# Performance work log

Measured on AMD Instinct MI355X. Metric: run time of the kernel, lower is better.

## Reference

```python
import jax, jax.numpy as jnp
import numpy as np

WEIGHTS = (0.5, 1.0, 2.0)   # per-channel weights (init kwarg)
INVERTED = True             # init kwarg


def setup_inputs() -> dict:
    key = jax.random.key(0)
    B, C, H, W = 16, 3, 256, 256
    # binary flood mask: nonzero = foreground (scipy EDT measures distance to nearest zero)
    flood = jax.random.randint(key, (B, C, H, W), 0, 2).astype(jnp.float32)
    return {"flood_batch": flood}


def _edt_squared(mask):
    """Exact squared Euclidean distance transform per [H,W] slice.

    mask: bool [B,C,H,W], True = foreground (nonzero). Returns float32 [B,C,H,W]
    squared distance from each True pixel to the nearest False pixel (0 at False).
    Uses the exact separable decomposition:
      D2[r,w] = min_{r'} ( g[r',w]^2 + (r-r')^2 ),  g = 1D horizontal distance to zero.
    """
    B, C, H, W = mask.shape
    BIG = jnp.float32(H + W)  # exceeds any achievable 1D distance

    # --- pass 1: 1D distance to nearest zero along W (forward + backward scans) ---
    m = jnp.moveaxis(mask, -1, 0)  # [W,B,C,H]

    def step(carry, mm):
        d = jnp.where(mm, jnp.minimum(carry + 1.0, BIG), 0.0)
        return d, d

    init = jnp.full((B, C, H), BIG, jnp.float32)
    _, fwd = jax.lax.scan(step, init, m)
    _, bwd = jax.lax.scan(step, init, m[::-1])
    g = jnp.minimum(fwd, bwd[::-1])          # [W,B,C,H]
    g2 = jnp.moveaxis(g, 0, -1) ** 2          # [B,C,H,W]

    # --- pass 2: exact min-plus over rows (vectorized over B,C,W; scan over output row) ---
    rows = jnp.arange(H, dtype=jnp.float32)

    def row_step(_, r):
        cand = g2 + ((r - rows) ** 2)[None, None, :, None]  # [B,C,H,W]
        return None, cand.min(axis=2)                        # [B,C,W]

    _, d2 = jax.lax.scan(row_step, None, rows)  # [H,B,C,W]
    return jnp.moveaxis(d2, 0, 2)               # [B,C,H,W]


def reference(flood_batch):
    w = jnp.asarray(WEIGHTS, jnp.float32)
    dt = jnp.sqrt(_edt_squared(flood_batch != 0))            # [B,C,H,W]
    dt = dt * w[None, :, None, None]                         # per-channel weight
    mx = dt.max(axis=(2, 3), keepdims=True)                  # per-slice max
    safe = jnp.where(mx > 0, mx, 1.0)
    scaled = (mx - dt) / safe if INVERTED else dt / safe
    return jnp.where(mx > 0, scaled, dt)
```

## Files before the change

kernel.cpp:

```cpp
#include <hip/hip_runtime.h>


#define BIGD 512.0f
#define PADV 1e30f

__global__ __launch_bounds__(256) void k1_bitmask(const float* __restrict__ in,
                                                  unsigned long long* __restrict__ bits) {
    int row = blockIdx.x * 4 + (threadIdx.x >> 6);
    int lane = threadIdx.x & 63;
    const float4 m = ((const float4*)in)[(long)row * 64 + lane];

    unsigned long long b0 = __ballot(m.x == 0.f);
    unsigned long long b1 = __ballot(m.y == 0.f);
    unsigned long long b2 = __ballot(m.z == 0.f);
    unsigned long long b3 = __ballot(m.w == 0.f);
    if (lane == 0) {
        ulonglong4* dst = (ulonglong4*)(bits + (long)row * 4);
        ulonglong4 v; v.x = b0; v.y = b1; v.z = b2; v.w = b3;
        *dst = v;
    }
}

__global__ __launch_bounds__(256) void k2_colpass(const unsigned long long* __restrict__ bits,
                                                  float* __restrict__ d2out,
                                                  float* __restrict__ stripmax) {
    __shared__ unsigned long long bm[1024];
    __shared__ float tile[16 * 289];
    __shared__ float wm[4];
    int bx = blockIdx.x;
    int slice = bx >> 4;
    int w0 = (bx & 15) * 16;
    int tid = threadIdx.x;

    {
        const unsigned long long* src = bits + (long)slice * 1024;
        #pragma unroll
        for (int i = 0; i < 4; ++i) bm[i * 256 + tid] = src[i * 256 + tid];
    }
    {
        int c = tid >> 4, i = tid & 15;
        tile[c * 289 + i] = PADV;
        tile[c * 289 + 272 + i] = PADV;
    }
    __syncthreads();

    int c = tid & 15;
    int p = w0 + c;
    int rg = tid >> 4;

    auto nz2 = [&](int row) -> float {
        int dist = 512;
        #pragma unroll
        for (int cc = 0; cc < 4; ++cc) {
            unsigned long long M = bm[row * 4 + cc];
            int q = p - cc;
            int qa = (q < 0) ? 0 : q;
            int tp = qa >> 2;
            unsigned long long Ml = (q >= 0) ? (M & (~0ull >> (63 - tp))) : 0ull;
            int tn = (q < 0) ? 0 : ((q + 3) >> 2);
            unsigned long long Mh = (tn < 64) ? (M & (~0ull << tn)) : 0ull;
            if (Ml) dist = min(dist, q - 4 * (63 - __builtin_clzll(Ml)));
            if (Mh) dist = min(dist, 4 * __builtin_ctzll(Mh) - q);
        }
        float fd = (float)dist;
        return fd * fd;
    };

    #pragma unroll
    for (int k = 0; k < 16; ++k) {
        int r = rg + 16 * k;
        tile[c * 289 + 16 + r] = nz2(r);
    }
    __syncthreads();

    int r0 = rg * 16;
    float s[48];
    #pragma unroll
    for (int i = 0; i < 48; ++i) s[i] = tile[c * 289 + r0 + i];

    float dmin[16];
    #pragma unroll
    for (int k = 0; k < 16; ++k) dmin[k] = s[k + 16];
    #pragma unroll
    for (int o = -16; o <= 16; ++o) {
        if (o == 0) continue;
        float oo = (float)(o * o);
        #pragma unroll
        for (int k = 0; k < 16; ++k)
            dmin[k] = fminf(dmin[k], s[k + 16 + o] + oo);
    }

    #pragma unroll
    for (int k = 0; k < 16; ++k) {
        if (dmin[k] > 288.0f) {
            float best = dmin[k];
            int r = r0 + k;
            for (int rp = 0; rp < 256; ++rp) {
                float dr = (float)(r - rp);
                best = fminf(best, fmaf(dr, dr, tile[c * 289 + 16 + rp]));
            }
            dmin[k] = best;
        }
    }

    float* dst = d2out + (long)slice * 65536 + w0 + c;
    float m = 0.f;
    #pragma unroll
    for (int k = 0; k < 16; ++k) {
        dst[(long)(r0 + k) * 256] = dmin[k];
        m = fmaxf(m, dmin[k]);
    }
    #pragma unroll
    for (int off = 32; off >= 1; off >>= 1)
        m = fmaxf(m, __shfl_down(m, off, 64));
    if ((tid & 63) == 0) wm[tid >> 6] = m;
    __syncthreads();
    if (tid == 0)
        stripmax[bx] = fmaxf(fmaxf(wm[0], wm[1]), fmaxf(wm[2], wm[3]));
}

__global__ __launch_bounds__(256) void k3_final(float* __restrict__ out,
                                                const float* __restrict__ stripmax) {
    __shared__ float sMx;
    int tid = threadIdx.x;
    int idx4 = blockIdx.x * 256 + tid;
    int slice = blockIdx.x >> 6;
    if (tid < 16) {
        float v = stripmax[slice * 16 + tid];
        #pragma unroll
        for (int off = 8; off >= 1; off >>= 1) v = fmaxf(v, __shfl_down(v, off, 64));
        if (tid == 0) sMx = v;
    }
    __syncthreads();

    int c = slice % 3;
    float wgt = (c == 0) ? 0.5f : ((c == 1) ? 1.0f : 2.0f);
    float mx = wgt * __builtin_sqrtf(sMx);

    float4 d2 = ((float4*)out)[idx4];
    float4 r;
    if (mx > 0.f) {
        float inv = 1.0f / mx;
        r.x = (mx - wgt * __builtin_sqrtf(d2.x)) * inv;
        r.y = (mx - wgt * __builtin_sqrtf(d2.y)) * inv;
        r.z = (mx - wgt * __builtin_sqrtf(d2.z)) * inv;
        r.w = (mx - wgt * __builtin_sqrtf(d2.w)) * inv;
    } else {
        r.x = wgt * __builtin_sqrtf(d2.x);
        r.y = wgt * __builtin_sqrtf(d2.y);
        r.z = wgt * __builtin_sqrtf(d2.z);
        r.w = wgt * __builtin_sqrtf(d2.w);
    }
    ((float4*)out)[idx4] = r;
}

extern "C" void kernel_launch(void* const* d_in, const int* in_sizes, int n_in,
                              void* d_out, int out_size, void* d_ws, size_t ws_size,
                              hipStream_t stream) {
    const float* in = (const float*)d_in[0];
    float* out = (float*)d_out;
    float* stripmax = (float*)d_ws;
    unsigned long long* bits = (unsigned long long*)((char*)d_ws + 4096);

    k1_bitmask<<<3072, 256, 0, stream>>>(in, bits);
    k2_colpass<<<768, 256, 0, stream>>>(bits, out, stripmax);
    k3_final<<<3072, 256, 0, stream>>>(out, stripmax);
}
```

Measured before the change: 83.01 us.

## Fuse column pass and normalization via cooperative grid sync

Merges the column min-plus kernel and the final normalization kernel into one cooperative kernel that keeps per-thread squared distances in registers, does a grid-wide sync after writing strip maxima, then writes normalized outputs directly. This removes a full intermediate write and read of the output buffer and one kernel launch. In exchange it needs all 768 blocks co-resident (launch bounds hint of 3 blocks per CU), adds grid sync latency, and holds 16 values per thread across the barrier, which raises register pressure.

```diff
diff --git a/kernel.cpp b/kernel.cpp
--- a/kernel.cpp
+++ b/kernel.cpp
@@ -1,7 +1,9 @@
 #include <hip/hip_runtime.h>
+#include <hip/hip_cooperative_groups.h>
+
+namespace cg = cooperative_groups;
 
 
-#define BIGD 512.0f
 #define PADV 1e30f
 
 __global__ __launch_bounds__(256) void k1_bitmask(const float* __restrict__ in,
@@ -21,12 +23,15 @@
     }
 }
 
-__global__ __launch_bounds__(256) void k2_colpass(const unsigned long long* __restrict__ bits,
-                                                  float* __restrict__ d2out,
-                                                  float* __restrict__ stripmax) {
+__global__ __launch_bounds__(256, 3) void k2_fused(const unsigned long long* __restrict__ bits,
+                                                   float* __restrict__ out,
+                                                   float* __restrict__ stripmax) {
     __shared__ unsigned long long bm[1024];
     __shared__ float tile[16 * 289];
     __shared__ float wm[4];
+    __shared__ float sMx;
+    cg::grid_group grid = cg::this_grid();
+
     int bx = blockIdx.x;
     int slice = bx >> 4;
     int w0 = (bx & 15) * 16;
@@ -103,13 +108,9 @@
         }
     }
 
-    float* dst = d2out + (long)slice * 65536 + w0 + c;
     float m = 0.f;
     #pragma unroll
-    for (int k = 0; k < 16; ++k) {
-        dst[(long)(r0 + k) * 256] = dmin[k];
-        m = fmaxf(m, dmin[k]);
-    }
+    for (int k = 0; k < 16; ++k) m = fmaxf(m, dmin[k]);
     #pragma unroll
     for (int off = 32; off >= 1; off >>= 1)
         m = fmaxf(m, __shfl_down(m, off, 64));
@@ -117,14 +118,9 @@
     __syncthreads();
     if (tid == 0)
         stripmax[bx] = fmaxf(fmaxf(wm[0], wm[1]), fmaxf(wm[2], wm[3]));
-}
 
-__global__ __launch_bounds__(256) void k3_final(float* __restrict__ out,
-                                                const float* __restrict__ stripmax) {
-    __shared__ float sMx;
-    int tid = threadIdx.x;
-    int idx4 = blockIdx.x * 256 + tid;
-    int slice = blockIdx.x >> 6;
+    grid.sync();
+
     if (tid < 16) {
         float v = stripmax[slice * 16 + tid];
         #pragma unroll
@@ -133,25 +129,21 @@
     }
     __syncthreads();
 
-    int c = slice % 3;
-    float wgt = (c == 0) ? 0.5f : ((c == 1) ? 1.0f : 2.0f);
+    int ch = slice % 3;
+    float wgt = (ch == 0) ? 0.5f : ((ch == 1) ? 1.0f : 2.0f);
     float mx = wgt * __builtin_sqrtf(sMx);
 
-    float4 d2 = ((float4*)out)[idx4];
-    float4 r;
+    float* dst = out + (long)slice * 65536 + w0 + c;
     if (mx > 0.f) {
         float inv = 1.0f / mx;
-        r.x = (mx - wgt * __builtin_sqrtf(d2.x)) * inv;
-        r.y = (mx - wgt * __builtin_sqrtf(d2.y)) * inv;
-        r.z = (mx - wgt * __builtin_sqrtf(d2.z)) * inv;
-        r.w = (mx - wgt * __builtin_sqrtf(d2.w)) * inv;
+        #pragma unroll
+        for (int k = 0; k < 16; ++k)
+            dst[(long)(r0 + k) * 256] = (mx - wgt * __builtin_sqrtf(dmin[k])) * inv;
     } else {
-        r.x = wgt * __builtin_sqrtf(d2.x);
-        r.y = wgt * __builtin_sqrtf(d2.y);
-        r.z = wgt * __builtin_sqrtf(d2.z);
-        r.w = wgt * __builtin_sqrtf(d2.w);
+        #pragma unroll
+        for (int k = 0; k < 16; ++k)
+            dst[(long)(r0 + k) * 256] = wgt * __builtin_sqrtf(dmin[k]);
     }
-    ((float4*)out)[idx4] = r;
 }
 
 extern "C" void kernel_launch(void* const* d_in, const int* in_sizes, int n_in,
@@ -163,6 +155,8 @@
     unsigned long long* bits = (unsigned long long*)((char*)d_ws + 4096);
 
     k1_bitmask<<<3072, 256, 0, stream>>>(in, bits);
-    k2_colpass<<<768, 256, 0, stream>>>(bits, out, stripmax);
-    k3_final<<<3072, 256, 0, stream>>>(out, stripmax);
+
+    void* args[] = { (void*)&bits, (void*)&out, (void*)&stripmax };
+    hipLaunchCooperativeKernel((const void*)k2_fused, dim3(768), dim3(256),
+                               args, 0, stream);
 }
```

New measurement: 128.3 us. 1.55x slower.
